# Optimization experiments

Hardware: AMD Instinct MI355X
Metric: run time of the kernel (lower is better)

## Reference

```python
import jax, jax.numpy as jnp
import numpy as np

SEQ, BATCH, IN, HID = 512, 64, 1024, 1024

def setup_inputs() -> dict:
    key = jax.random.key(0)
    k0, k1, k2, k3, k4 = jax.random.split(key, 5)
    k = 1.0 / np.sqrt(HID).astype(np.float32)
    x = jax.random.normal(k0, (SEQ, BATCH, IN), dtype=jnp.float32)
    W_ih = jax.random.uniform(k1, (HID, IN), jnp.float32, -k, k)
    W_hh = jax.random.uniform(k2, (HID, HID), jnp.float32, -k, k)
    b_ih = jax.random.uniform(k3, (HID,), jnp.float32, -k, k)
    b_hh = jax.random.uniform(k4, (HID,), jnp.float32, -k, k)
    return {"x": x, "W_ih": W_ih, "W_hh": W_hh, "b_ih": b_ih, "b_hh": b_hh}

def reference(x, W_ih, W_hh, b_ih, b_hh):
    # Elman RNN: h_t = tanh(x_t @ W_ih^T + h_{t-1} @ W_hh^T + b_ih + b_hh)
    B = x.shape[1]
    H = W_hh.shape[0]
    # Precompute all input projections in one big GEMM: [S,B,H]
    xW = jnp.einsum('sbi,hi->sbh', x, W_ih) + (b_ih + b_hh)
    W_hh_T = W_hh.T
    def step(h, xw_t):
        h_new = jnp.tanh(xw_t + h @ W_hh_T)
        return h_new, h_new
    h0 = jnp.zeros((B, H), dtype=x.dtype)
    h_last, out = jax.lax.scan(step, h0, xW)
    # output: [S,B,H]; h_n: [1,B,H]
    return out, h_last[None, :, :]
```

## Files before the change

### kernel.cpp

```cpp
#include <hip/hip_runtime.h>

typedef short short8 __attribute__((ext_vector_type(8)));
typedef float f32x4 __attribute__((ext_vector_type(4)));
typedef unsigned short us4 __attribute__((ext_vector_type(4)));

#define SQ 512
#define BA 64
#define HD 1024
#define NWG 64

__device__ __forceinline__ unsigned short f2bf(float f) {
    unsigned u = __float_as_uint(f);
    u += 0x7fffu + ((u >> 16) & 1u);
    return (unsigned short)(u >> 16);
}
__device__ __forceinline__ float bf2f(unsigned short h) {
    return __uint_as_float(((unsigned)h) << 16);
}
__device__ __forceinline__ void waitcnt_vm0() {
    asm volatile("s_waitcnt vmcnt(0)" ::: "memory");
}
__device__ __forceinline__ short8 ld_frag(const unsigned short* p) {
    const unsigned long long* q = (const unsigned long long*)p;
    unsigned long long a = __hip_atomic_load(q,     __ATOMIC_RELAXED, __HIP_MEMORY_SCOPE_AGENT);
    unsigned long long b = __hip_atomic_load(q + 1, __ATOMIC_RELAXED, __HIP_MEMORY_SCOPE_AGENT);
    union { unsigned long long u[2]; short8 v; } cv;
    cv.u[0] = a; cv.u[1] = b;
    return cv.v;
}

__global__ void __launch_bounds__(256) xw_gemm(
    const float* __restrict__ x, const float* __restrict__ Wih,
    const float* __restrict__ bih, const float* __restrict__ bhh,
    float* __restrict__ out, unsigned* __restrict__ flags)
{
    if (blockIdx.x == 0 && blockIdx.y == 0)
        flags[threadIdx.x] = 0u;

    __shared__ unsigned short Ahi[128][40];
    __shared__ unsigned short Alo[128][40];
    __shared__ unsigned short Bhi[128][40];
    __shared__ unsigned short Blo[128][40];

    const int tid  = threadIdx.x;
    const int lane = tid & 63, wid = tid >> 6;
    const int bx = blockIdx.x, by = blockIdx.y;
    const int wm = (wid & 1) * 64, wn = (wid >> 1) * 64;
    const int rf = lane & 15, bq = lane >> 4, kf = bq * 8;

    f32x4 acc[4][4] = {};

    const int srow = tid >> 3;
    const int scol = (tid & 7) * 4;
    const float* aBase = x   + (size_t)(bx * 128 + srow) * HD + scol;
    const float* bBase = Wih + (size_t)(by * 128 + srow) * HD + scol;

    for (int kc = 0; kc < 32; ++kc) {
        __syncthreads();
        const int ko = kc * 32;
#pragma unroll
        for (int i = 0; i < 4; ++i) {
            const int r = srow + i * 32;
            float4 av = *(const float4*)(aBase + (size_t)(i * 32) * HD + ko);
            float4 bv = *(const float4*)(bBase + (size_t)(i * 32) * HD + ko);
            us4 ah, al, bh, bl;
            ah.x = f2bf(av.x); al.x = f2bf(av.x - bf2f(ah.x));
            ah.y = f2bf(av.y); al.y = f2bf(av.y - bf2f(ah.y));
            ah.z = f2bf(av.z); al.z = f2bf(av.z - bf2f(ah.z));
            ah.w = f2bf(av.w); al.w = f2bf(av.w - bf2f(ah.w));
            bh.x = f2bf(bv.x); bl.x = f2bf(bv.x - bf2f(bh.x));
            bh.y = f2bf(bv.y); bl.y = f2bf(bv.y - bf2f(bh.y));
            bh.z = f2bf(bv.z); bl.z = f2bf(bv.z - bf2f(bh.z));
            bh.w = f2bf(bv.w); bl.w = f2bf(bv.w - bf2f(bh.w));
            *(us4*)&Ahi[r][scol] = ah;
            *(us4*)&Alo[r][scol] = al;
            *(us4*)&Bhi[r][scol] = bh;
            *(us4*)&Blo[r][scol] = bl;
        }
        __syncthreads();

        short8 afh[4], afl[4], bfh[4], bfl[4];
#pragma unroll
        for (int i = 0; i < 4; ++i) {
            afh[i] = *(const short8*)&Ahi[wm + 16 * i + rf][kf];
            afl[i] = *(const short8*)&Alo[wm + 16 * i + rf][kf];
            bfh[i] = *(const short8*)&Bhi[wn + 16 * i + rf][kf];
            bfl[i] = *(const short8*)&Blo[wn + 16 * i + rf][kf];
        }
#pragma unroll
        for (int i = 0; i < 4; ++i)
#pragma unroll
            for (int j = 0; j < 4; ++j) {
                acc[i][j] = __builtin_amdgcn_mfma_f32_16x16x32_bf16(afh[i], bfh[j], acc[i][j], 0, 0, 0);
                acc[i][j] = __builtin_amdgcn_mfma_f32_16x16x32_bf16(afh[i], bfl[j], acc[i][j], 0, 0, 0);
                acc[i][j] = __builtin_amdgcn_mfma_f32_16x16x32_bf16(afl[i], bfh[j], acc[i][j], 0, 0, 0);
            }
    }

#pragma unroll
    for (int j = 0; j < 4; ++j) {
        const int col = by * 128 + wn + 16 * j + rf;
        const float bias = bih[col] + bhh[col];
#pragma unroll
        for (int i = 0; i < 4; ++i) {
            const int row0 = bx * 128 + wm + 16 * i + bq * 4;
#pragma unroll
            for (int r = 0; r < 4; ++r)
                out[(size_t)(row0 + r) * HD + col] = acc[i][j][r] + bias;
        }
    }
}

__global__ void __launch_bounds__(256, 1) rnn_recurrence(
    const float* __restrict__ Whh,
    float* __restrict__ io,
    float* __restrict__ hn,
    unsigned short* __restrict__ hbuf,
    unsigned* __restrict__ flags)
{
    __shared__ unsigned short Whi[16][1032];
    __shared__ unsigned short Wlo[16][1032];

    const int tid = threadIdx.x;
    const int bx  = blockIdx.x;
    const int h0  = bx * 16;

    for (int i = tid; i < 16 * 1024; i += 256) {
        const int r = i >> 10, c = i & 1023;
        const float w = Whh[(size_t)(h0 + r) * HD + c];
        const unsigned short hi = f2bf(w);
        Whi[r][c] = hi;
        Wlo[r][c] = f2bf(w - bf2f(hi));
    }
    __syncthreads();

    const int lane = tid & 63, wid = tid >> 6;
    const int rf = lane & 15, bq = lane >> 4, kf = bq * 8;

    unsigned short* H0 = hbuf;
    unsigned short* H1 = hbuf + BA * HD;

    const int brow = wid * 16 + bq * 4;
    const int col  = h0 + rf;
    const int ab   = wid * 16 + rf;

    unsigned*       myflag = flags + wid * 64 + bx;
    const unsigned* watch  = flags + wid * 64 + lane;

    float v[4];
    unsigned hi4[4];
    float xwv[4];

#pragma unroll
    for (int r = 0; r < 4; ++r) {
        v[r] = tanhf(io[(size_t)(brow + r) * HD + col]);
        hi4[r] = f2bf(v[r]);
    }
#pragma unroll
    for (int r = 0; r < 4; ++r) {
        const unsigned oh = __shfl_xor(hi4[r], 1);
        if ((lane & 1) == 0) {
            const size_t e = ((size_t)(brow + r) * HD + col) >> 1;
            __hip_atomic_store((unsigned*)H0 + e, (hi4[r] & 0xffffu) | (oh << 16),
                               __ATOMIC_RELAXED, __HIP_MEMORY_SCOPE_AGENT);
        }
        io[(size_t)(brow + r) * HD + col] = v[r];
    }
    waitcnt_vm0();
    if (lane == 0)
        __hip_atomic_store(myflag, 1u, __ATOMIC_RELAXED, __HIP_MEMORY_SCOPE_AGENT);

#pragma unroll
    for (int r = 0; r < 4; ++r)
        xwv[r] = io[(size_t)(BA * HD) + (size_t)(brow + r) * HD + col];

    for (int t = 1; t < SQ; ++t) {
        unsigned fv = __hip_atomic_load(watch, __ATOMIC_RELAXED, __HIP_MEMORY_SCOPE_AGENT);
        while (!__all((int)(fv >= (unsigned)t)))
            fv = __hip_atomic_load(watch, __ATOMIC_RELAXED, __HIP_MEMORY_SCOPE_AGENT);

        const unsigned short* Ph = (t & 1) ? H0 : H1;
        unsigned short*       Nh = (t & 1) ? H1 : H0;
        const unsigned short* ap = Ph + (size_t)ab * HD + kf;

        short8 a[32];
#pragma unroll
        for (int kc = 0; kc < 32; ++kc)
            a[kc] = ld_frag(ap + (size_t)kc * 32);

        float xwn[4] = {0.f, 0.f, 0.f, 0.f};
        if (t + 1 < SQ) {
            const float* nxt = io + (size_t)(t + 1) * (BA * HD);
#pragma unroll
            for (int r = 0; r < 4; ++r)
                xwn[r] = nxt[(size_t)(brow + r) * HD + col];
        }

        f32x4 ah0 = {}, ah1 = {}, al0 = {}, al1 = {};
#pragma unroll
        for (int kc = 0; kc < 32; ++kc) {
            short8 bh = *(const short8*)&Whi[rf][kc * 32 + kf];
            short8 bl = *(const short8*)&Wlo[rf][kc * 32 + kf];
            if (kc & 1) {
                ah1 = __builtin_amdgcn_mfma_f32_16x16x32_bf16(a[kc], bh, ah1, 0, 0, 0);
                al1 = __builtin_amdgcn_mfma_f32_16x16x32_bf16(a[kc], bl, al1, 0, 0, 0);
            } else {
                ah0 = __builtin_amdgcn_mfma_f32_16x16x32_bf16(a[kc], bh, ah0, 0, 0, 0);
                al0 = __builtin_amdgcn_mfma_f32_16x16x32_bf16(a[kc], bl, al0, 0, 0, 0);
            }
        }

#pragma unroll
        for (int r = 0; r < 4; ++r) {
            v[r] = tanhf(((ah0[r] + ah1[r]) + (al0[r] + al1[r])) + xwv[r]);
            hi4[r] = f2bf(v[r]);
            xwv[r] = xwn[r];
        }

        if (t < SQ - 1) {
            float* outP = io + (size_t)t * (BA * HD);
#pragma unroll
            for (int r = 0; r < 4; ++r) {
                const unsigned oh = __shfl_xor(hi4[r], 1);
                if ((lane & 1) == 0) {
                    const size_t e = ((size_t)(brow + r) * HD + col) >> 1;
                    __hip_atomic_store((unsigned*)Nh + e, (hi4[r] & 0xffffu) | (oh << 16),
                                       __ATOMIC_RELAXED, __HIP_MEMORY_SCOPE_AGENT);
                }
                outP[(size_t)(brow + r) * HD + col] = v[r];
            }
            waitcnt_vm0();
            if (lane == 0)
                __hip_atomic_store(myflag, (unsigned)(t + 1),
                                   __ATOMIC_RELAXED, __HIP_MEMORY_SCOPE_AGENT);
        }
    }

    float* outL = io + (size_t)(SQ - 1) * (BA * HD);
#pragma unroll
    for (int r = 0; r < 4; ++r) {
        const size_t o = (size_t)(brow + r) * HD + col;
        outL[o] = v[r];
        hn[o]   = v[r];
    }
}

extern "C" void kernel_launch(void* const* d_in, const int* in_sizes, int n_in,
                              void* d_out, int out_size, void* d_ws, size_t ws_size,
                              hipStream_t stream) {
    const float* x   = (const float*)d_in[0];
    const float* Wih = (const float*)d_in[1];
    const float* Whh = (const float*)d_in[2];
    const float* bih = (const float*)d_in[3];
    const float* bhh = (const float*)d_in[4];

    float* io = (float*)d_out;
    float* hn = io + (size_t)SQ * BA * HD;

    unsigned* flags = (unsigned*)d_ws;
    unsigned short* hbuf = (unsigned short*)((char*)d_ws + 4096);

    hipLaunchKernelGGL(xw_gemm, dim3(256, 8), dim3(256), 0, stream,
                       x, Wih, bih, bhh, io, flags);

    void* args[] = {(void*)&Whh, (void*)&io, (void*)&hn, (void*)&hbuf, (void*)&flags};
    hipLaunchCooperativeKernel((void*)rnn_recurrence, dim3(NWG), dim3(256),
                               args, 0, stream);
}
```

Measured before the change: 5.628 ms.

## Halve recurrence workgroups to 32, each computing 32 hidden columns

The persistent recurrence kernel now runs 32 workgroups instead of 64, each holding 32 rows of W_hh (hi/lo bf16 splits) in LDS and issuing twice the MFMAs per step. Fewer participants means fewer flags to poll per step, which shrinks the cross-workgroup barrier cost. The output and next-xW global accesses move after the flag publish so they leave the critical path, and s_sleep is added to the spin loop to ease polling pressure. In exchange, per-step compute per workgroup doubles, LDS use doubles to about 132KB, and the work is spread over fewer CUs.

```diff
diff --git a/kernel.cpp b/kernel.cpp
--- a/kernel.cpp
+++ b/kernel.cpp
@@ -7,7 +7,7 @@
 #define SQ 512
 #define BA 64
 #define HD 1024
-#define NWG 64
+#define NWG 32
 
 __device__ __forceinline__ unsigned short f2bf(float f) {
     unsigned u = __float_as_uint(f);
@@ -34,7 +34,7 @@
     const float* __restrict__ bih, const float* __restrict__ bhh,
     float* __restrict__ out, unsigned* __restrict__ flags)
 {
-    if (blockIdx.x == 0 && blockIdx.y == 0)
+    if (blockIdx.x == 0 && blockIdx.y == 0 && threadIdx.x < 128)
         flags[threadIdx.x] = 0u;
 
     __shared__ unsigned short Ahi[128][40];
@@ -118,14 +118,14 @@
     unsigned short* __restrict__ hbuf,
     unsigned* __restrict__ flags)
 {
-    __shared__ unsigned short Whi[16][1032];
-    __shared__ unsigned short Wlo[16][1032];
+    __shared__ unsigned short Whi[32][1032];
+    __shared__ unsigned short Wlo[32][1032];
 
     const int tid = threadIdx.x;
     const int bx  = blockIdx.x;
-    const int h0  = bx * 16;
-
-    for (int i = tid; i < 16 * 1024; i += 256) {
+    const int h0  = bx * 32;
+
+    for (int i = tid; i < 32 * 1024; i += 256) {
         const int r = i >> 10, c = i & 1023;
         const float w = Whh[(size_t)(h0 + r) * HD + c];
         const unsigned short hi = f2bf(w);
@@ -141,43 +141,55 @@
     unsigned short* H1 = hbuf + BA * HD;
 
     const int brow = wid * 16 + bq * 4;
-    const int col  = h0 + rf;
     const int ab   = wid * 16 + rf;
-
-    unsigned*       myflag = flags + wid * 64 + bx;
-    const unsigned* watch  = flags + wid * 64 + lane;
-
-    float v[4];
-    unsigned hi4[4];
-    float xwv[4];
-
-#pragma unroll
-    for (int r = 0; r < 4; ++r) {
-        v[r] = tanhf(io[(size_t)(brow + r) * HD + col]);
-        hi4[r] = f2bf(v[r]);
-    }
-#pragma unroll
-    for (int r = 0; r < 4; ++r) {
-        const unsigned oh = __shfl_xor(hi4[r], 1);
-        if ((lane & 1) == 0) {
-            const size_t e = ((size_t)(brow + r) * HD + col) >> 1;
-            __hip_atomic_store((unsigned*)H0 + e, (hi4[r] & 0xffffu) | (oh << 16),
-                               __ATOMIC_RELAXED, __HIP_MEMORY_SCOPE_AGENT);
-        }
-        io[(size_t)(brow + r) * HD + col] = v[r];
-    }
+    const int col0 = h0 + rf;
+
+    unsigned*       myflag = flags + wid * 32 + bx;
+    const unsigned* watch  = flags + wid * 32 + (lane & 31);
+
+    float v[2][4];
+    unsigned hi4[2][4];
+    float xwv[2][4];
+
+#pragma unroll
+    for (int j = 0; j < 2; ++j)
+#pragma unroll
+        for (int r = 0; r < 4; ++r) {
+            v[j][r] = tanhf(io[(size_t)(brow + r) * HD + col0 + 16 * j]);
+            hi4[j][r] = f2bf(v[j][r]);
+        }
+#pragma unroll
+    for (int j = 0; j < 2; ++j)
+#pragma unroll
+        for (int r = 0; r < 4; ++r) {
+            const unsigned oh = __shfl_xor(hi4[j][r], 1);
+            if ((lane & 1) == 0) {
+                const size_t e = ((size_t)(brow + r) * HD + col0 + 16 * j) >> 1;
+                __hip_atomic_store((unsigned*)H0 + e, (hi4[j][r] & 0xffffu) | (oh << 16),
+                                   __ATOMIC_RELAXED, __HIP_MEMORY_SCOPE_AGENT);
+            }
+        }
     waitcnt_vm0();
     if (lane == 0)
         __hip_atomic_store(myflag, 1u, __ATOMIC_RELAXED, __HIP_MEMORY_SCOPE_AGENT);
 
 #pragma unroll
-    for (int r = 0; r < 4; ++r)
-        xwv[r] = io[(size_t)(BA * HD) + (size_t)(brow + r) * HD + col];
+    for (int j = 0; j < 2; ++j)
+#pragma unroll
+        for (int r = 0; r < 4; ++r)
+            io[(size_t)(brow + r) * HD + col0 + 16 * j] = v[j][r];
+#pragma unroll
+    for (int j = 0; j < 2; ++j)
+#pragma unroll
+        for (int r = 0; r < 4; ++r)
+            xwv[j][r] = io[(size_t)(BA * HD) + (size_t)(brow + r) * HD + col0 + 16 * j];
 
     for (int t = 1; t < SQ; ++t) {
         unsigned fv = __hip_atomic_load(watch, __ATOMIC_RELAXED, __HIP_MEMORY_SCOPE_AGENT);
-        while (!__all((int)(fv >= (unsigned)t)))
+        while (!__all((int)(fv >= (unsigned)t))) {
+            __builtin_amdgcn_s_sleep(1);
             fv = __hip_atomic_load(watch, __ATOMIC_RELAXED, __HIP_MEMORY_SCOPE_AGENT);
+        }
 
         const unsigned short* Ph = (t & 1) ? H0 : H1;
         unsigned short*       Nh = (t & 1) ? H1 : H0;
@@ -188,61 +200,73 @@
         for (int kc = 0; kc < 32; ++kc)
             a[kc] = ld_frag(ap + (size_t)kc * 32);
 
-        float xwn[4] = {0.f, 0.f, 0.f, 0.f};
-        if (t + 1 < SQ) {
-            const float* nxt = io + (size_t)(t + 1) * (BA * HD);
-#pragma unroll
-            for (int r = 0; r < 4; ++r)
-                xwn[r] = nxt[(size_t)(brow + r) * HD + col];
-        }
-
-        f32x4 ah0 = {}, ah1 = {}, al0 = {}, al1 = {};
+        f32x4 c0h0 = {}, c0h1 = {}, c0l0 = {}, c0l1 = {};
+        f32x4 c1h0 = {}, c1h1 = {}, c1l0 = {}, c1l1 = {};
 #pragma unroll
         for (int kc = 0; kc < 32; ++kc) {
-            short8 bh = *(const short8*)&Whi[rf][kc * 32 + kf];
-            short8 bl = *(const short8*)&Wlo[rf][kc * 32 + kf];
+            short8 b0h = *(const short8*)&Whi[rf][kc * 32 + kf];
+            short8 b0l = *(const short8*)&Wlo[rf][kc * 32 + kf];
+            short8 b1h = *(const short8*)&Whi[16 + rf][kc * 32 + kf];
+            short8 b1l = *(const short8*)&Wlo[16 + rf][kc * 32 + kf];
             if (kc & 1) {
-                ah1 = __builtin_amdgcn_mfma_f32_16x16x32_bf16(a[kc], bh, ah1, 0, 0, 0);
-                al1 = __builtin_amdgcn_mfma_f32_16x16x32_bf16(a[kc], bl, al1, 0, 0, 0);
+                c0h1 = __builtin_amdgcn_mfma_f32_16x16x32_bf16(a[kc], b0h, c0h1, 0, 0, 0);
+                c0l1 = __builtin_amdgcn_mfma_f32_16x16x32_bf16(a[kc], b0l, c0l1, 0, 0, 0);
+                c1h1 = __builtin_amdgcn_mfma_f32_16x16x32_bf16(a[kc], b1h, c1h1, 0, 0, 0);
+                c1l1 = __builtin_amdgcn_mfma_f32_16x16x32_bf16(a[kc], b1l, c1l1, 0, 0, 0);
             } else {
-                ah0 = __builtin_amdgcn_mfma_f32_16x16x32_bf16(a[kc], bh, ah0, 0, 0, 0);
-                al0 = __builtin_amdgcn_mfma_f32_16x16x32_bf16(a[kc], bl, al0, 0, 0, 0);
+                c0h0 = __builtin_amdgcn_mfma_f32_16x16x32_bf16(a[kc], b0h, c0h0, 0, 0, 0);
+                c0l0 = __builtin_amdgcn_mfma_f32_16x16x32_bf16(a[kc], b0l, c0l0, 0, 0, 0);
+                c1h0 = __builtin_amdgcn_mfma_f32_16x16x32_bf16(a[kc], b1h, c1h0, 0, 0, 0);
+                c1l0 = __builtin_amdgcn_mfma_f32_16x16x32_bf16(a[kc], b1l, c1l0, 0, 0, 0);
             }
         }
 
 #pragma unroll
         for (int r = 0; r < 4; ++r) {
-            v[r] = tanhf(((ah0[r] + ah1[r]) + (al0[r] + al1[r])) + xwv[r]);
-            hi4[r] = f2bf(v[r]);
-            xwv[r] = xwn[r];
+            v[0][r] = tanhf(((c0h0[r] + c0h1[r]) + (c0l0[r] + c0l1[r])) + xwv[0][r]);
+            v[1][r] = tanhf(((c1h0[r] + c1h1[r]) + (c1l0[r] + c1l1[r])) + xwv[1][r]);
+            hi4[0][r] = f2bf(v[0][r]);
+            hi4[1][r] = f2bf(v[1][r]);
         }
 
         if (t < SQ - 1) {
-            float* outP = io + (size_t)t * (BA * HD);
-#pragma unroll
-            for (int r = 0; r < 4; ++r) {
-                const unsigned oh = __shfl_xor(hi4[r], 1);
-                if ((lane & 1) == 0) {
-                    const size_t e = ((size_t)(brow + r) * HD + col) >> 1;
-                    __hip_atomic_store((unsigned*)Nh + e, (hi4[r] & 0xffffu) | (oh << 16),
-                                       __ATOMIC_RELAXED, __HIP_MEMORY_SCOPE_AGENT);
+#pragma unroll
+            for (int j = 0; j < 2; ++j)
+#pragma unroll
+                for (int r = 0; r < 4; ++r) {
+                    const unsigned oh = __shfl_xor(hi4[j][r], 1);
+                    if ((lane & 1) == 0) {
+                        const size_t e = ((size_t)(brow + r) * HD + col0 + 16 * j) >> 1;
+                        __hip_atomic_store((unsigned*)Nh + e, (hi4[j][r] & 0xffffu) | (oh << 16),
+                                           __ATOMIC_RELAXED, __HIP_MEMORY_SCOPE_AGENT);
+                    }
                 }
-                outP[(size_t)(brow + r) * HD + col] = v[r];
-            }
             waitcnt_vm0();
             if (lane == 0)
                 __hip_atomic_store(myflag, (unsigned)(t + 1),
                                    __ATOMIC_RELAXED, __HIP_MEMORY_SCOPE_AGENT);
+
+            float* outP = io + (size_t)t * (BA * HD);
+            const float* nxt = io + (size_t)(t + 1) * (BA * HD);
+#pragma unroll
+            for (int j = 0; j < 2; ++j)
+#pragma unroll
+                for (int r = 0; r < 4; ++r) {
+                    outP[(size_t)(brow + r) * HD + col0 + 16 * j] = v[j][r];
+                    xwv[j][r] = nxt[(size_t)(brow + r) * HD + col0 + 16 * j];
+                }
         }
     }
 
     float* outL = io + (size_t)(SQ - 1) * (BA * HD);
 #pragma unroll
-    for (int r = 0; r < 4; ++r) {
-        const size_t o = (size_t)(brow + r) * HD + col;
-        outL[o] = v[r];
-        hn[o]   = v[r];
-    }
+    for (int j = 0; j < 2; ++j)
+#pragma unroll
+        for (int r = 0; r < 4; ++r) {
+            const size_t o = (size_t)(brow + r) * HD + col0 + 16 * j;
+            outL[o] = v[j][r];
+            hn[o]   = v[j][r];
+        }
 }
 
 extern "C" void kernel_launch(void* const* d_in, const int* in_sizes, int n_in,
```

Result: faster. 5.473 ms (-2.7%).
